# Performance work log

Measured on AMD Instinct MI355X. Metric: run time of the kernel, lower is better.

Reference implementation:

```python
import jax, jax.numpy as jnp
import numpy as np

N_NODES = 100_000
N_EDGES = 1_600_000
N_RELS = 16
D_IN = 128
D_OUT = 64


def setup_inputs() -> dict:
    key = jax.random.key(0)
    k_feat, k_w, k_src, k_dst, k_et = jax.random.split(key, 5)
    feat = jax.random.normal(k_feat, (N_NODES, D_IN), dtype=jnp.float32)
    weight = jax.random.normal(k_w, (N_RELS, D_IN, D_OUT), dtype=jnp.float32)
    src = jax.random.randint(k_src, (N_EDGES,), 0, N_NODES, dtype=jnp.int32)
    dst = jax.random.randint(k_dst, (N_EDGES,), 0, N_NODES, dtype=jnp.int32)
    etypes = jnp.sort(jax.random.randint(k_et, (N_EDGES,), 0, N_RELS, dtype=jnp.int32))
    return {"feat": feat, "weight": weight, "src": src, "dst": dst, "etypes": etypes}


def reference(feat, weight, src, dst, etypes):
    # RGCN gather-mm: message m_e = feat[src_e] @ W[etype_e]; out_v = sum_{e: dst_e = v} m_e
    # Efficient form: project all nodes with all relation weights (dense GEMM, small R),
    # then gather the (etype, src) slice per edge and segment-sum into destinations.
    proj = jnp.einsum('nd,rde->rne', feat, weight)          # [R, N, d_out]
    msg = proj[etypes, src]                                  # [E, d_out] irregular gather
    out = jax.ops.segment_sum(msg, dst, num_segments=feat.shape[0])  # [N, d_out] scatter-sum
    return out
```

## Files before the change

kernel.cpp:

```cpp
#include <hip/hip_runtime.h>
#include <hip/hip_bf16.h>


#define NTHREADS 256
#define TM 64

typedef __attribute__((ext_vector_type(8))) __bf16 bf16x8;
typedef __attribute__((ext_vector_type(4))) float f32x4;

__global__ void cvt_w_kernel(const float* __restrict__ w,
                             __bf16* __restrict__ o, int total) {
    int idx = blockIdx.x * 256 + threadIdx.x;
    if (idx >= total) return;
    int r = idx >> 13;
    int rem = idx & 8191;
    int k = rem >> 6;
    int n = rem & 63;
    o[(r << 13) + (n << 7) + k] = (__bf16)w[idx];
}

__global__ __launch_bounds__(NTHREADS)
void proj_all_kernel(const float* __restrict__ feat, const __bf16* __restrict__ wtb,
                     const unsigned char* __restrict__ usedb,
                     int N, int R, __bf16* __restrict__ projb) {
    __shared__ __bf16 Wt[2][64 * 136];
    __shared__ unsigned used_l[16 * 32];

    int t = threadIdx.x;
    int wave = t >> 6, lane = t & 63;
    int q = lane >> 4, m = lane & 15;
    long blk0 = (long)blockIdx.x * 128;
    long node0 = blk0 + wave * 32;

    for (int c = t; c < R * 32; c += NTHREADS) {
        int rr = c >> 5, i = c & 31;
        used_l[rr * 32 + i] = *(const unsigned*)(usedb + (size_t)rr * N + blk0 + i * 4);
    }

    bf16x8 a[2][4];
    #pragma unroll
    for (int mt = 0; mt < 2; mt++) {
        long nd = node0 + mt * 16 + m;
        if (nd > N - 1) nd = N - 1;
        const float* arow = feat + nd * 128;
        #pragma unroll
        for (int ks = 0; ks < 4; ks++) {
            float4 fa = *(const float4*)(arow + ks * 32 + q * 8);
            float4 fb = *(const float4*)(arow + ks * 32 + q * 8 + 4);
            bf16x8 v;
            v[0] = (__bf16)fa.x; v[1] = (__bf16)fa.y; v[2] = (__bf16)fa.z; v[3] = (__bf16)fa.w;
            v[4] = (__bf16)fb.x; v[5] = (__bf16)fb.y; v[6] = (__bf16)fb.z; v[7] = (__bf16)fb.w;
            a[mt][ks] = v;
        }
    }

    {
        const __bf16* wg = wtb;
        #pragma unroll
        for (int i = 0; i < 4; i++) {
            int c = t + i * 256;
            int n = c >> 4, kc = c & 15;
            *(bf16x8*)(&Wt[0][n * 136 + kc * 8]) = *(const bf16x8*)(wg + n * 128 + kc * 8);
        }
    }
    asm volatile("s_waitcnt lgkmcnt(0)" ::: "memory");
    __builtin_amdgcn_s_barrier();
    __builtin_amdgcn_sched_barrier(0);

    for (int r = 0; r < R; r++) {
        int cur = r & 1, nxt = cur ^ 1;
        bool pf = (r + 1 < R);

        bf16x8 wreg[4];
        if (pf) {
            const __bf16* wg = wtb + ((size_t)(r + 1) << 13);
            #pragma unroll
            for (int i = 0; i < 4; i++) {
                int c = t + i * 256;
                int n = c >> 4, kc = c & 15;
                wreg[i] = *(const bf16x8*)(wg + n * 128 + kc * 8);
            }
        }

        f32x4 acc[2][4] = {};
        #pragma unroll
        for (int ks = 0; ks < 4; ks++) {
            bf16x8 b0 = *(const bf16x8*)(&Wt[cur][(0 * 16 + m) * 136 + ks * 32 + q * 8]);
            bf16x8 b1 = *(const bf16x8*)(&Wt[cur][(1 * 16 + m) * 136 + ks * 32 + q * 8]);
            bf16x8 b2 = *(const bf16x8*)(&Wt[cur][(2 * 16 + m) * 136 + ks * 32 + q * 8]);
            bf16x8 b3 = *(const bf16x8*)(&Wt[cur][(3 * 16 + m) * 136 + ks * 32 + q * 8]);
            #pragma unroll
            for (int mt = 0; mt < 2; mt++) {
                acc[mt][0] = __builtin_amdgcn_mfma_f32_16x16x32_bf16(a[mt][ks], b0, acc[mt][0], 0, 0, 0);
                acc[mt][1] = __builtin_amdgcn_mfma_f32_16x16x32_bf16(a[mt][ks], b1, acc[mt][1], 0, 0, 0);
                acc[mt][2] = __builtin_amdgcn_mfma_f32_16x16x32_bf16(a[mt][ks], b2, acc[mt][2], 0, 0, 0);
                acc[mt][3] = __builtin_amdgcn_mfma_f32_16x16x32_bf16(a[mt][ks], b3, acc[mt][3], 0, 0, 0);
            }
        }

        #pragma unroll
        for (int mt = 0; mt < 2; mt++) {
            unsigned g = used_l[r * 32 + ((wave * 32 + mt * 16 + q * 4) >> 2)];
            #pragma unroll
            for (int reg = 0; reg < 4; reg++) {
                long nd = node0 + mt * 16 + q * 4 + reg;
                if (nd < N && ((g >> (reg * 8)) & 1)) {
                    union { unsigned long long u; __bf16 h[4]; } pk;
                    pk.h[0] = (__bf16)acc[mt][0][reg];
                    pk.h[1] = (__bf16)acc[mt][1][reg];
                    pk.h[2] = (__bf16)acc[mt][2][reg];
                    pk.h[3] = (__bf16)acc[mt][3][reg];
                    *(unsigned long long*)(projb + ((size_t)r * N + nd) * 64 + m * 4) = pk.u;
                }
            }
        }

        if (pf) {
            #pragma unroll
            for (int i = 0; i < 4; i++) {
                int c = t + i * 256;
                int n = c >> 4, kc = c & 15;
                *(bf16x8*)(&Wt[nxt][n * 136 + kc * 8]) = wreg[i];
            }
            asm volatile("s_waitcnt lgkmcnt(0)" ::: "memory");
            __builtin_amdgcn_s_barrier();
            __builtin_amdgcn_sched_barrier(0);
        }
    }
}

__global__ __launch_bounds__(1024)
void bucket_hist(const int* __restrict__ dst, int E, int* __restrict__ bhist) {
    __shared__ int lh[1024];
    int t = threadIdx.x;
    lh[t] = 0;
    __syncthreads();
    long base = (long)blockIdx.x * 8192;
    #pragma unroll
    for (int i = 0; i < 8; i++) {
        long e = base + t + 1024 * i;
        if (e < E) atomicAdd(&lh[dst[e] >> 7], 1);
    }
    __syncthreads();
    if (lh[t]) atomicAdd(&bhist[t], lh[t]);
}

__global__ __launch_bounds__(1024)
void bucket_scan(const int* __restrict__ bhist, int NB, int N, int E,
                 int* __restrict__ boff, int* __restrict__ bcur,
                 int* __restrict__ dofs) {
    __shared__ int sm[1024];
    int t = threadIdx.x;
    int v = (t < NB) ? bhist[t] : 0;
    sm[t] = v;
    __syncthreads();
    for (int s = 1; s < 1024; s <<= 1) {
        int add = (t >= s) ? sm[t - s] : 0;
        __syncthreads();
        sm[t] += add;
        __syncthreads();
    }
    if (t < NB) { int ex = sm[t] - v; boff[t] = ex; bcur[t] = ex; }
    if (t == 0) { boff[NB] = E; dofs[N] = E; }
}

__global__ __launch_bounds__(1024)
void bucket_scatter(const int* __restrict__ dst, const int* __restrict__ src,
                    const int* __restrict__ etypes, int E, int N, int NB,
                    int* __restrict__ bcur, int* __restrict__ items,
                    unsigned char* __restrict__ usedb) {
    __shared__ int lh[1024], lb[1024];
    int t = threadIdx.x;
    lh[t] = 0;
    __syncthreads();
    long base = (long)blockIdx.x * 8192;
    int bs[8], it[8];
    #pragma unroll
    for (int i = 0; i < 8; i++) {
        long e = base + t + 1024 * i;
        if (e < E) {
            int d = dst[e];
            int bkt = d >> 7;
            bs[i] = bkt;
            int pair = etypes[e] * N + src[e];
            it[i] = ((d & 127) << 24) | pair;
            usedb[pair] = 1;
            atomicAdd(&lh[bkt], 1);
        } else bs[i] = -1;
    }
    __syncthreads();
    for (int bb = t; bb < NB; bb += 1024) {
        int c = lh[bb];
        lb[bb] = c ? atomicAdd(&bcur[bb], c) : 0;
        lh[bb] = 0;
    }
    __syncthreads();
    #pragma unroll
    for (int i = 0; i < 8; i++) {
        if (bs[i] >= 0) {
            int pos = lb[bs[i]] + atomicAdd(&lh[bs[i]], 1);
            items[pos] = it[i];
        }
    }
}

__global__ __launch_bounds__(256)
void refine_kernel(const int* __restrict__ boff, const int* __restrict__ items,
                   int N, int* __restrict__ pidx, int* __restrict__ dofs) {
    __shared__ int h[128], sc[128], cur[128];
    int b = blockIdx.x, t = threadIdx.x;
    int j0 = boff[b], j1 = boff[b + 1];
    if (t < 128) h[t] = 0;
    __syncthreads();
    for (int j = j0 + t; j < j1; j += 256)
        atomicAdd(&h[((unsigned)items[j]) >> 24], 1);
    __syncthreads();
    if (t < 128) sc[t] = h[t];
    __syncthreads();
    for (int s = 1; s < 128; s <<= 1) {
        int add = (t >= s && t < 128) ? sc[t - s] : 0;
        __syncthreads();
        if (t < 128) sc[t] += add;
        __syncthreads();
    }
    if (t < 128) {
        int ex = sc[t] - h[t];
        cur[t] = ex;
        int v = (b << 7) + t;
        if (v < N) dofs[v] = j0 + ex;
    }
    __syncthreads();
    for (int j = j0 + t; j < j1; j += 256) {
        int it = items[j];
        int dl = ((unsigned)it) >> 24;
        int pos = j0 + atomicAdd(&cur[dl], 1);
        pidx[pos] = it & 0xFFFFFF;
    }
}

__global__ __launch_bounds__(256)
void reduce_kernel(const int* __restrict__ dofs, const int* __restrict__ pidx,
                   const __bf16* __restrict__ projb, int N, float* __restrict__ out) {
    int gid = blockIdx.x * 256 + threadIdx.x;
    int w = gid >> 6, lane = gid & 63;
    int nw = (gridDim.x * 256) >> 6;
    int sub = lane >> 3, c8 = lane & 7;
    for (int v = w; v < N; v += nw) {
        int j0 = dofs[v], j1 = dofs[v + 1];
        float acc[8] = {0.f, 0.f, 0.f, 0.f, 0.f, 0.f, 0.f, 0.f};
        for (int j = j0 + sub; j < j1; j += 8) {
            int p = pidx[j];
            bf16x8 val = *(const bf16x8*)(projb + (size_t)p * 64 + c8 * 8);
            #pragma unroll
            for (int i = 0; i < 8; i++) acc[i] += (float)val[i];
        }
        #pragma unroll
        for (int mask = 8; mask <= 32; mask <<= 1) {
            #pragma unroll
            for (int i = 0; i < 8; i++) acc[i] += __shfl_xor(acc[i], mask, 64);
        }
        if (sub == 0) {
            float* orow = out + (size_t)v * 64;
            #pragma unroll
            for (int i = 0; i < 8; i++) {
                int cp = c8 * 8 + i;
                orow[(cp & 3) * 16 + (cp >> 2)] = acc[i];
            }
        }
    }
}

__global__ __launch_bounds__(NTHREADS)
void rgcn_atomic(const float* __restrict__ feat, const float* __restrict__ weight,
                 const int* __restrict__ src, const int* __restrict__ dst,
                 const int* __restrict__ etypes, int E,
                 float* __restrict__ out) {
    __shared__ __bf16 Wt[64 * 136];
    int b = blockIdx.x;
    int e0 = b * TM;
    int t = threadIdx.x;
    int wave = t >> 6, lane = t & 63;
    int q = lane >> 4, m = lane & 15;
    int wbase = e0 + wave * 16;
    int last = e0 + TM - 1; if (last > E - 1) last = E - 1;
    int rmin = etypes[e0];
    int rmax = etypes[last];
    int em = wbase + m;
    bool rowok = em < E;
    int ei = rowok ? em : E - 1;
    int my_et = rowok ? etypes[em] : -1;
    const float* arow = feat + (long)src[ei] * 128;
    bf16x8 a[4];
    #pragma unroll
    for (int ks = 0; ks < 4; ks++) {
        float4 fa = *(const float4*)(arow + ks * 32 + q * 8);
        float4 fb = *(const float4*)(arow + ks * 32 + q * 8 + 4);
        bf16x8 v;
        v[0] = (__bf16)fa.x; v[1] = (__bf16)fa.y;
        v[2] = (__bf16)fa.z; v[3] = (__bf16)fa.w;
        v[4] = (__bf16)fb.x; v[5] = (__bf16)fb.y;
        v[6] = (__bf16)fb.z; v[7] = (__bf16)fb.w;
        a[ks] = v;
    }
    f32x4 acc0 = {0.f, 0.f, 0.f, 0.f};
    f32x4 acc1 = {0.f, 0.f, 0.f, 0.f};
    f32x4 acc2 = {0.f, 0.f, 0.f, 0.f};
    f32x4 acc3 = {0.f, 0.f, 0.f, 0.f};
    for (int r = rmin; r <= rmax; ++r) {
        if (r != rmin) __syncthreads();
        const float* wg = weight + (r << 13);
        for (int p = t; p < 4096; p += NTHREADS) {
            int n = p & 63, kh = p >> 6;
            float w0 = wg[(kh * 2) * 64 + n];
            float w1 = wg[(kh * 2 + 1) * 64 + n];
            union { unsigned u; __bf16 h[2]; } pk;
            pk.h[0] = (__bf16)w0; pk.h[1] = (__bf16)w1;
            *(unsigned*)&Wt[n * 136 + kh * 2] = pk.u;
        }
        __syncthreads();
        bool on = (my_et == r);
        #pragma unroll
        for (int ks = 0; ks < 4; ks++) {
            bf16x8 af = a[ks];
            if (!on) {
                #pragma unroll
                for (int j = 0; j < 8; j++) af[j] = (__bf16)0.f;
            }
            bf16x8 b0 = *(const bf16x8*)(&Wt[(0 * 16 + m) * 136 + ks * 32 + q * 8]);
            bf16x8 b1 = *(const bf16x8*)(&Wt[(1 * 16 + m) * 136 + ks * 32 + q * 8]);
            bf16x8 b2 = *(const bf16x8*)(&Wt[(2 * 16 + m) * 136 + ks * 32 + q * 8]);
            bf16x8 b3 = *(const bf16x8*)(&Wt[(3 * 16 + m) * 136 + ks * 32 + q * 8]);
            acc0 = __builtin_amdgcn_mfma_f32_16x16x32_bf16(af, b0, acc0, 0, 0, 0);
            acc1 = __builtin_amdgcn_mfma_f32_16x16x32_bf16(af, b1, acc1, 0, 0, 0);
            acc2 = __builtin_amdgcn_mfma_f32_16x16x32_bf16(af, b2, acc2, 0, 0, 0);
            acc3 = __builtin_amdgcn_mfma_f32_16x16x32_bf16(af, b3, acc3, 0, 0, 0);
        }
    }
    #pragma unroll
    for (int reg = 0; reg < 4; reg++) {
        int er = wbase + q * 4 + reg;
        if (er < E) {
            float* orow = out + (long)dst[er] * 64;
            unsafeAtomicAdd(orow + 0 * 16 + m, acc0[reg]);
            unsafeAtomicAdd(orow + 1 * 16 + m, acc1[reg]);
            unsafeAtomicAdd(orow + 2 * 16 + m, acc2[reg]);
            unsafeAtomicAdd(orow + 3 * 16 + m, acc3[reg]);
        }
    }
}

extern "C" void kernel_launch(void* const* d_in, const int* in_sizes, int n_in,
                              void* d_out, int out_size, void* d_ws, size_t ws_size,
                              hipStream_t stream) {
    const float* feat   = (const float*)d_in[0];
    const float* weight = (const float*)d_in[1];
    const int*   src    = (const int*)d_in[2];
    const int*   dst    = (const int*)d_in[3];
    const int*   etypes = (const int*)d_in[4];
    float* out = (float*)d_out;

    int nfeat = in_sizes[0];
    int nw    = in_sizes[1];
    int E     = in_sizes[2];
    int N     = nfeat / 128;
    int R     = nw >> 13;
    int NB    = (N + 127) >> 7;

    size_t o = 0;
    auto take = [&](size_t bytes) { size_t r = o; o = (o + bytes + 255) & ~(size_t)255; return r; };
    size_t o_bhist = take((size_t)NB * 4);
    size_t o_usedb = take((size_t)R * N);
    size_t o_boff  = take((size_t)(NB + 1) * 4);
    size_t o_bcur  = take((size_t)NB * 4);
    size_t o_dofs  = take((size_t)(N + 1) * 4);
    size_t o_items = take((size_t)E * 4);
    size_t o_pidx  = take((size_t)E * 4);
    size_t o_wtb   = take((size_t)nw * 2);
    size_t o_projb = take((size_t)R * N * 64 * 2);
    size_t need = o;

    bool fast = (ws_size >= need) && (NB <= 1024) && ((size_t)R * N < (1u << 24)) && (R <= 16);

    if (fast) {
        char* ws = (char*)d_ws;
        int* bhist = (int*)(ws + o_bhist);
        unsigned char* usedb = (unsigned char*)(ws + o_usedb);
        int* boff  = (int*)(ws + o_boff);
        int* bcur  = (int*)(ws + o_bcur);
        int* dofs  = (int*)(ws + o_dofs);
        int* items = (int*)(ws + o_items);
        int* pidx  = (int*)(ws + o_pidx);
        __bf16* wtb   = (__bf16*)(ws + o_wtb);
        __bf16* projb = (__bf16*)(ws + o_projb);

        int cgrid = (int)(((long)E + 8191) / 8192);

        hipMemsetAsync(bhist, 0, (size_t)NB * 4, stream);
        hipMemsetAsync(usedb, 0, (size_t)R * N, stream);
        bucket_hist<<<cgrid, 1024, 0, stream>>>(dst, E, bhist);
        bucket_scan<<<1, 1024, 0, stream>>>(bhist, NB, N, E, boff, bcur, dofs);
        bucket_scatter<<<cgrid, 1024, 0, stream>>>(dst, src, etypes, E, N, NB, bcur, items, usedb);
        refine_kernel<<<NB, 256, 0, stream>>>(boff, items, N, pidx, dofs);
        cvt_w_kernel<<<(nw + 255) / 256, 256, 0, stream>>>(weight, wtb, nw);

        proj_all_kernel<<<(N + 127) / 128, NTHREADS, 0, stream>>>(feat, wtb, usedb, N, R, projb);
        reduce_kernel<<<2048, 256, 0, stream>>>(dofs, pidx, projb, N, out);
    } else {
        hipMemsetAsync(d_out, 0, (size_t)out_size * sizeof(float), stream);
        int mgrid = (E + TM - 1) / TM;
        rgcn_atomic<<<mgrid, NTHREADS, 0, stream>>>(feat, weight, src, dst, etypes, E, out);
    }
}
```

Baseline: 256.3 us.

## Split projection kernel across relations, one block per node tile and relation

The projection kernel no longer loops over all relations inside one block with double-buffered weight tiles. It now launches one block per (node tile, relation) pair, so each block loads a single weight slice and computes one small GEMM. This gives R times more blocks for better occupancy and latency hiding, but each feature row is now read and converted once per relation instead of once. A guard requiring N divisible by 4 is added to the fast path.

```diff
diff --git a/kernel.cpp b/kernel.cpp
--- a/kernel.cpp
+++ b/kernel.cpp
@@ -20,22 +20,32 @@
 }
 
 __global__ __launch_bounds__(NTHREADS)
-void proj_all_kernel(const float* __restrict__ feat, const __bf16* __restrict__ wtb,
+void proj_rel_kernel(const float* __restrict__ feat, const __bf16* __restrict__ wtb,
                      const unsigned char* __restrict__ usedb,
                      int N, int R, __bf16* __restrict__ projb) {
-    __shared__ __bf16 Wt[2][64 * 136];
-    __shared__ unsigned used_l[16 * 32];
+    __shared__ __bf16 Wt[64 * 136];
+    __shared__ unsigned used_l[32];
+
+    int bid = blockIdx.x;
+    int r = bid % R;
+    long xt = bid / R;
 
     int t = threadIdx.x;
     int wave = t >> 6, lane = t & 63;
     int q = lane >> 4, m = lane & 15;
-    long blk0 = (long)blockIdx.x * 128;
+    long blk0 = xt * 128;
     long node0 = blk0 + wave * 32;
 
-    for (int c = t; c < R * 32; c += NTHREADS) {
-        int rr = c >> 5, i = c & 31;
-        used_l[rr * 32 + i] = *(const unsigned*)(usedb + (size_t)rr * N + blk0 + i * 4);
-    }
+    {
+        const __bf16* wg = wtb + ((size_t)r << 13);
+        #pragma unroll
+        for (int i = 0; i < 4; i++) {
+            int c = t + i * 256;
+            int n = c >> 4, kc = c & 15;
+            *(bf16x8*)(&Wt[n * 136 + kc * 8]) = *(const bf16x8*)(wg + n * 128 + kc * 8);
+        }
+    }
+    if (t < 32) used_l[t] = *(const unsigned*)(usedb + (size_t)r * N + blk0 + t * 4);
 
     bf16x8 a[2][4];
     #pragma unroll
@@ -54,77 +64,38 @@
         }
     }
 
-    {
-        const __bf16* wg = wtb;
-        #pragma unroll
-        for (int i = 0; i < 4; i++) {
-            int c = t + i * 256;
-            int n = c >> 4, kc = c & 15;
-            *(bf16x8*)(&Wt[0][n * 136 + kc * 8]) = *(const bf16x8*)(wg + n * 128 + kc * 8);
-        }
-    }
-    asm volatile("s_waitcnt lgkmcnt(0)" ::: "memory");
-    __builtin_amdgcn_s_barrier();
-    __builtin_amdgcn_sched_barrier(0);
-
-    for (int r = 0; r < R; r++) {
-        int cur = r & 1, nxt = cur ^ 1;
-        bool pf = (r + 1 < R);
-
-        bf16x8 wreg[4];
-        if (pf) {
-            const __bf16* wg = wtb + ((size_t)(r + 1) << 13);
-            #pragma unroll
-            for (int i = 0; i < 4; i++) {
-                int c = t + i * 256;
-                int n = c >> 4, kc = c & 15;
-                wreg[i] = *(const bf16x8*)(wg + n * 128 + kc * 8);
+    __syncthreads();
+
+    f32x4 acc[2][4] = {};
+    #pragma unroll
+    for (int ks = 0; ks < 4; ks++) {
+        bf16x8 b0 = *(const bf16x8*)(&Wt[(0 * 16 + m) * 136 + ks * 32 + q * 8]);
+        bf16x8 b1 = *(const bf16x8*)(&Wt[(1 * 16 + m) * 136 + ks * 32 + q * 8]);
+        bf16x8 b2 = *(const bf16x8*)(&Wt[(2 * 16 + m) * 136 + ks * 32 + q * 8]);
+        bf16x8 b3 = *(const bf16x8*)(&Wt[(3 * 16 + m) * 136 + ks * 32 + q * 8]);
+        #pragma unroll
+        for (int mt = 0; mt < 2; mt++) {
+            acc[mt][0] = __builtin_amdgcn_mfma_f32_16x16x32_bf16(a[mt][ks], b0, acc[mt][0], 0, 0, 0);
+            acc[mt][1] = __builtin_amdgcn_mfma_f32_16x16x32_bf16(a[mt][ks], b1, acc[mt][1], 0, 0, 0);
+            acc[mt][2] = __builtin_amdgcn_mfma_f32_16x16x32_bf16(a[mt][ks], b2, acc[mt][2], 0, 0, 0);
+            acc[mt][3] = __builtin_amdgcn_mfma_f32_16x16x32_bf16(a[mt][ks], b3, acc[mt][3], 0, 0, 0);
+        }
+    }
+
+    #pragma unroll
+    for (int mt = 0; mt < 2; mt++) {
+        unsigned g = used_l[wave * 8 + mt * 4 + q];
+        #pragma unroll
+        for (int reg = 0; reg < 4; reg++) {
+            long nd = node0 + mt * 16 + q * 4 + reg;
+            if (nd < N && ((g >> (reg * 8)) & 1)) {
+                union { unsigned long long u; __bf16 h[4]; } pk;
+                pk.h[0] = (__bf16)acc[mt][0][reg];
+                pk.h[1] = (__bf16)acc[mt][1][reg];
+                pk.h[2] = (__bf16)acc[mt][2][reg];
+                pk.h[3] = (__bf16)acc[mt][3][reg];
+                *(unsigned long long*)(projb + ((size_t)r * N + nd) * 64 + m * 4) = pk.u;
             }
-        }
-
-        f32x4 acc[2][4] = {};
-        #pragma unroll
-        for (int ks = 0; ks < 4; ks++) {
-            bf16x8 b0 = *(const bf16x8*)(&Wt[cur][(0 * 16 + m) * 136 + ks * 32 + q * 8]);
-            bf16x8 b1 = *(const bf16x8*)(&Wt[cur][(1 * 16 + m) * 136 + ks * 32 + q * 8]);
-            bf16x8 b2 = *(const bf16x8*)(&Wt[cur][(2 * 16 + m) * 136 + ks * 32 + q * 8]);
-            bf16x8 b3 = *(const bf16x8*)(&Wt[cur][(3 * 16 + m) * 136 + ks * 32 + q * 8]);
-            #pragma unroll
-            for (int mt = 0; mt < 2; mt++) {
-                acc[mt][0] = __builtin_amdgcn_mfma_f32_16x16x32_bf16(a[mt][ks], b0, acc[mt][0], 0, 0, 0);
-                acc[mt][1] = __builtin_amdgcn_mfma_f32_16x16x32_bf16(a[mt][ks], b1, acc[mt][1], 0, 0, 0);
-                acc[mt][2] = __builtin_amdgcn_mfma_f32_16x16x32_bf16(a[mt][ks], b2, acc[mt][2], 0, 0, 0);
-                acc[mt][3] = __builtin_amdgcn_mfma_f32_16x16x32_bf16(a[mt][ks], b3, acc[mt][3], 0, 0, 0);
-            }
-        }
-
-        #pragma unroll
-        for (int mt = 0; mt < 2; mt++) {
-            unsigned g = used_l[r * 32 + ((wave * 32 + mt * 16 + q * 4) >> 2)];
-            #pragma unroll
-            for (int reg = 0; reg < 4; reg++) {
-                long nd = node0 + mt * 16 + q * 4 + reg;
-                if (nd < N && ((g >> (reg * 8)) & 1)) {
-                    union { unsigned long long u; __bf16 h[4]; } pk;
-                    pk.h[0] = (__bf16)acc[mt][0][reg];
-                    pk.h[1] = (__bf16)acc[mt][1][reg];
-                    pk.h[2] = (__bf16)acc[mt][2][reg];
-                    pk.h[3] = (__bf16)acc[mt][3][reg];
-                    *(unsigned long long*)(projb + ((size_t)r * N + nd) * 64 + m * 4) = pk.u;
-                }
-            }
-        }
-
-        if (pf) {
-            #pragma unroll
-            for (int i = 0; i < 4; i++) {
-                int c = t + i * 256;
-                int n = c >> 4, kc = c & 15;
-                *(bf16x8*)(&Wt[nxt][n * 136 + kc * 8]) = wreg[i];
-            }
-            asm volatile("s_waitcnt lgkmcnt(0)" ::: "memory");
-            __builtin_amdgcn_s_barrier();
-            __builtin_amdgcn_sched_barrier(0);
         }
     }
 }
@@ -379,7 +350,8 @@
     size_t o_projb = take((size_t)R * N * 64 * 2);
     size_t need = o;
 
-    bool fast = (ws_size >= need) && (NB <= 1024) && ((size_t)R * N < (1u << 24)) && (R <= 16);
+    bool fast = (ws_size >= need) && (NB <= 1024) && ((size_t)R * N < (1u << 24))
+                && (R <= 16) && ((N & 3) == 0);
 
     if (fast) {
         char* ws = (char*)d_ws;
@@ -403,7 +375,8 @@
         refine_kernel<<<NB, 256, 0, stream>>>(boff, items, N, pidx, dofs);
         cvt_w_kernel<<<(nw + 255) / 256, 256, 0, stream>>>(weight, wtb, nw);
 
-        proj_all_kernel<<<(N + 127) / 128, NTHREADS, 0, stream>>>(feat, wtb, usedb, N, R, projb);
+        int nblk = ((N + 127) / 128) * R;
+        proj_rel_kernel<<<nblk, NTHREADS, 0, stream>>>(feat, wtb, usedb, N, R, projb);
         reduce_kernel<<<2048, 256, 0, stream>>>(dofs, pidx, projb, N, out);
     } else {
         hipMemsetAsync(d_out, 0, (size_t)out_size * sizeof(float), stream);
```

New measurement: 311.1 us. +21.3%, slower.

## Replace CSR build with fixed-stride buckets and LDS-atomic bucket reduction

Applied to the files above, without the earlier changes.

Drops the histogram, scan and refine passes. Edges are scattered directly into fixed-capacity per-bucket slots using atomic counters. A new per-bucket reduce kernel accumulates messages into a 128x64 shared-memory tile with float atomics and writes the tile out. This removes several launches and global passes over the edge list. In exchange it relies on bucket counts not exceeding STRIDE (overflow is silently dropped) and on LDS atomic throughput.

```diff
diff --git a/kernel.cpp b/kernel.cpp
--- a/kernel.cpp
+++ b/kernel.cpp
@@ -130,44 +130,9 @@
 }
 
 __global__ __launch_bounds__(1024)
-void bucket_hist(const int* __restrict__ dst, int E, int* __restrict__ bhist) {
-    __shared__ int lh[1024];
-    int t = threadIdx.x;
-    lh[t] = 0;
-    __syncthreads();
-    long base = (long)blockIdx.x * 8192;
-    #pragma unroll
-    for (int i = 0; i < 8; i++) {
-        long e = base + t + 1024 * i;
-        if (e < E) atomicAdd(&lh[dst[e] >> 7], 1);
-    }
-    __syncthreads();
-    if (lh[t]) atomicAdd(&bhist[t], lh[t]);
-}
-
-__global__ __launch_bounds__(1024)
-void bucket_scan(const int* __restrict__ bhist, int NB, int N, int E,
-                 int* __restrict__ boff, int* __restrict__ bcur,
-                 int* __restrict__ dofs) {
-    __shared__ int sm[1024];
-    int t = threadIdx.x;
-    int v = (t < NB) ? bhist[t] : 0;
-    sm[t] = v;
-    __syncthreads();
-    for (int s = 1; s < 1024; s <<= 1) {
-        int add = (t >= s) ? sm[t - s] : 0;
-        __syncthreads();
-        sm[t] += add;
-        __syncthreads();
-    }
-    if (t < NB) { int ex = sm[t] - v; boff[t] = ex; bcur[t] = ex; }
-    if (t == 0) { boff[NB] = E; dofs[N] = E; }
-}
-
-__global__ __launch_bounds__(1024)
 void bucket_scatter(const int* __restrict__ dst, const int* __restrict__ src,
-                    const int* __restrict__ etypes, int E, int N, int NB,
-                    int* __restrict__ bcur, int* __restrict__ items,
+                    const int* __restrict__ etypes, int E, int N, int NB, int STRIDE,
+                    int* __restrict__ bcnt, int* __restrict__ items,
                     unsigned char* __restrict__ usedb) {
     __shared__ int lh[1024], lb[1024];
     int t = threadIdx.x;
@@ -191,7 +156,7 @@
     __syncthreads();
     for (int bb = t; bb < NB; bb += 1024) {
         int c = lh[bb];
-        lb[bb] = c ? atomicAdd(&bcur[bb], c) : 0;
+        lb[bb] = c ? atomicAdd(&bcnt[bb], c) : 0;
         lh[bb] = 0;
     }
     __syncthreads();
@@ -199,73 +164,43 @@
     for (int i = 0; i < 8; i++) {
         if (bs[i] >= 0) {
             int pos = lb[bs[i]] + atomicAdd(&lh[bs[i]], 1);
-            items[pos] = it[i];
-        }
-    }
-}
-
-__global__ __launch_bounds__(256)
-void refine_kernel(const int* __restrict__ boff, const int* __restrict__ items,
-                   int N, int* __restrict__ pidx, int* __restrict__ dofs) {
-    __shared__ int h[128], sc[128], cur[128];
+            if (pos < STRIDE)
+                items[(size_t)bs[i] * STRIDE + pos] = it[i];
+        }
+    }
+}
+
+__global__ __launch_bounds__(512)
+void bucket_reduce(const int* __restrict__ bcnt, const int* __restrict__ items,
+                   int STRIDE, const __bf16* __restrict__ projb, int N,
+                   float* __restrict__ out) {
+    __shared__ float accl[128 * 64];
     int b = blockIdx.x, t = threadIdx.x;
-    int j0 = boff[b], j1 = boff[b + 1];
-    if (t < 128) h[t] = 0;
-    __syncthreads();
-    for (int j = j0 + t; j < j1; j += 256)
-        atomicAdd(&h[((unsigned)items[j]) >> 24], 1);
-    __syncthreads();
-    if (t < 128) sc[t] = h[t];
-    __syncthreads();
-    for (int s = 1; s < 128; s <<= 1) {
-        int add = (t >= s && t < 128) ? sc[t - s] : 0;
-        __syncthreads();
-        if (t < 128) sc[t] += add;
-        __syncthreads();
-    }
-    if (t < 128) {
-        int ex = sc[t] - h[t];
-        cur[t] = ex;
-        int v = (b << 7) + t;
-        if (v < N) dofs[v] = j0 + ex;
-    }
-    __syncthreads();
-    for (int j = j0 + t; j < j1; j += 256) {
-        int it = items[j];
+    int cnt = bcnt[b]; if (cnt > STRIDE) cnt = STRIDE;
+    const int* bitems = items + (size_t)b * STRIDE;
+
+    for (int i = t; i < 8192; i += 512) accl[i] = 0.f;
+    __syncthreads();
+
+    int team = t >> 3, c8 = t & 7;
+    for (int k = team; k < cnt; k += 64) {
+        int it = bitems[k];
         int dl = ((unsigned)it) >> 24;
-        int pos = j0 + atomicAdd(&cur[dl], 1);
-        pidx[pos] = it & 0xFFFFFF;
-    }
-}
-
-__global__ __launch_bounds__(256)
-void reduce_kernel(const int* __restrict__ dofs, const int* __restrict__ pidx,
-                   const __bf16* __restrict__ projb, int N, float* __restrict__ out) {
-    int gid = blockIdx.x * 256 + threadIdx.x;
-    int w = gid >> 6, lane = gid & 63;
-    int nw = (gridDim.x * 256) >> 6;
-    int sub = lane >> 3, c8 = lane & 7;
-    for (int v = w; v < N; v += nw) {
-        int j0 = dofs[v], j1 = dofs[v + 1];
-        float acc[8] = {0.f, 0.f, 0.f, 0.f, 0.f, 0.f, 0.f, 0.f};
-        for (int j = j0 + sub; j < j1; j += 8) {
-            int p = pidx[j];
-            bf16x8 val = *(const bf16x8*)(projb + (size_t)p * 64 + c8 * 8);
-            #pragma unroll
-            for (int i = 0; i < 8; i++) acc[i] += (float)val[i];
-        }
-        #pragma unroll
-        for (int mask = 8; mask <= 32; mask <<= 1) {
-            #pragma unroll
-            for (int i = 0; i < 8; i++) acc[i] += __shfl_xor(acc[i], mask, 64);
-        }
-        if (sub == 0) {
-            float* orow = out + (size_t)v * 64;
-            #pragma unroll
-            for (int i = 0; i < 8; i++) {
-                int cp = c8 * 8 + i;
-                orow[(cp & 3) * 16 + (cp >> 2)] = acc[i];
-            }
+        int p  = it & 0xFFFFFF;
+        bf16x8 v = *(const bf16x8*)(projb + (size_t)p * 64 + c8 * 8);
+        float* ab = accl + dl * 64 + c8 * 8;
+        #pragma unroll
+        for (int i = 0; i < 8; i++) atomicAdd(&ab[i], (float)v[i]);
+    }
+    __syncthreads();
+
+    long v0 = (long)b * 128;
+    for (int idx = t; idx < 8192; idx += 512) {
+        int vloc = idx >> 6, ca = idx & 63;
+        long v = v0 + vloc;
+        if (v < N) {
+            int cp = ((ca & 15) << 2) | (ca >> 4);
+            out[(size_t)v * 64 + ca] = accl[vloc * 64 + cp];
         }
     }
 }
@@ -366,15 +301,15 @@
     int R     = nw >> 13;
     int NB    = (N + 127) >> 7;
 
+    int avg = (int)(((long)E + NB - 1) / NB);
+    int STRIDE = ((avg * 2 + 63) / 64) * 64;
+    if (STRIDE < 1024) STRIDE = 1024;
+
     size_t o = 0;
     auto take = [&](size_t bytes) { size_t r = o; o = (o + bytes + 255) & ~(size_t)255; return r; };
-    size_t o_bhist = take((size_t)NB * 4);
+    size_t o_bcnt  = take((size_t)NB * 4);
     size_t o_usedb = take((size_t)R * N);
-    size_t o_boff  = take((size_t)(NB + 1) * 4);
-    size_t o_bcur  = take((size_t)NB * 4);
-    size_t o_dofs  = take((size_t)(N + 1) * 4);
-    size_t o_items = take((size_t)E * 4);
-    size_t o_pidx  = take((size_t)E * 4);
+    size_t o_items = take((size_t)NB * STRIDE * 4);
     size_t o_wtb   = take((size_t)nw * 2);
     size_t o_projb = take((size_t)R * N * 64 * 2);
     size_t need = o;
@@ -383,28 +318,21 @@
 
     if (fast) {
         char* ws = (char*)d_ws;
-        int* bhist = (int*)(ws + o_bhist);
+        int* bcnt  = (int*)(ws + o_bcnt);
         unsigned char* usedb = (unsigned char*)(ws + o_usedb);
-        int* boff  = (int*)(ws + o_boff);
-        int* bcur  = (int*)(ws + o_bcur);
-        int* dofs  = (int*)(ws + o_dofs);
         int* items = (int*)(ws + o_items);
-        int* pidx  = (int*)(ws + o_pidx);
         __bf16* wtb   = (__bf16*)(ws + o_wtb);
         __bf16* projb = (__bf16*)(ws + o_projb);
 
         int cgrid = (int)(((long)E + 8191) / 8192);
 
-        hipMemsetAsync(bhist, 0, (size_t)NB * 4, stream);
-        hipMemsetAsync(usedb, 0, (size_t)R * N, stream);
-        bucket_hist<<<cgrid, 1024, 0, stream>>>(dst, E, bhist);
-        bucket_scan<<<1, 1024, 0, stream>>>(bhist, NB, N, E, boff, bcur, dofs);
-        bucket_scatter<<<cgrid, 1024, 0, stream>>>(dst, src, etypes, E, N, NB, bcur, items, usedb);
-        refine_kernel<<<NB, 256, 0, stream>>>(boff, items, N, pidx, dofs);
+        hipMemsetAsync(bcnt, 0, (o_usedb - o_bcnt) + (size_t)R * N, stream);
+        bucket_scatter<<<cgrid, 1024, 0, stream>>>(dst, src, etypes, E, N, NB, STRIDE,
+                                                   bcnt, items, usedb);
         cvt_w_kernel<<<(nw + 255) / 256, 256, 0, stream>>>(weight, wtb, nw);
 
         proj_all_kernel<<<(N + 127) / 128, NTHREADS, 0, stream>>>(feat, wtb, usedb, N, R, projb);
-        reduce_kernel<<<2048, 256, 0, stream>>>(dofs, pidx, projb, N, out);
+        bucket_reduce<<<NB, 512, 0, stream>>>(bcnt, items, STRIDE, projb, N, out);
     } else {
         hipMemsetAsync(d_out, 0, (size_t)out_size * sizeof(float), stream);
         int mgrid = (E + TM - 1) / TM;
```

New measurement: 862.8 us. 3.37x slower.
